# Performance work log

Measured on AMD Instinct MI355X. Metric: run time of the kernel, lower is better.

The kernel has to match this reference:

```python
import jax, jax.numpy as jnp
import numpy as np

FF = 7    # feature_filter_size
FC = 3    # feature_channel_size
PF = 9    # patch_filter_size
R = 9     # search_radius


def setup_inputs() -> dict:
    key = jax.random.key(0)
    x = jax.random.uniform(key, (1, 384, 384, 3), dtype=jnp.float32)
    # feature filter initialized as in the module: identity delta at center per color
    ff = np.zeros((FF, FF, 3, FC), np.float32)
    c = FF // 2
    for i in range(3):
        ff[c, c, i, i] = 1.0
    pf = np.ones((PF, PF), np.float32)   # patch filter = all ones (box)
    inv_sigma = jnp.ones((1,), jnp.float32)
    return {"x": x,
            "feature_filter": jnp.asarray(ff),
            "patch_filter": jnp.asarray(pf),
            "inv_sigma": inv_sigma}


def _conv_same_edge(img, kern):
    # img [B,H,W,Ci], kern [kh,kw,Ci,Co]; edge-clamped boundary (Halide clamp)
    kh, kw = kern.shape[0], kern.shape[1]
    ph, pw = kh // 2, kw // 2
    p = jnp.pad(img, ((0, 0), (ph, ph), (pw, pw), (0, 0)), mode="edge")
    return jax.lax.conv_general_dilated(
        p, kern, window_strides=(1, 1), padding="VALID",
        dimension_numbers=("NHWC", "HWIO", "NHWC"))


def reference(x, feature_filter, patch_filter, inv_sigma):
    B, H, W, C = x.shape
    fc = feature_filter.shape[-1]
    # 1) learned feature transform of the image
    feat = _conv_same_edge(x, feature_filter)                    # [B,H,W,FC]
    # edge-clamped padded copies for shifted (search-window) reads
    xp = jnp.pad(x,    ((0, 0), (R, R), (R, R), (0, 0)), mode="edge")
    fp = jnp.pad(feat, ((0, 0), (R, R), (R, R), (0, 0)), mode="edge")
    pk = patch_filter[:, :, None, None]                          # [PF,PF,1,1]

    dys, dxs = jnp.meshgrid(jnp.arange(2 * R + 1), jnp.arange(2 * R + 1), indexing="ij")
    offsets = jnp.stack([dys.ravel(), dxs.ravel()], axis=-1)     # [(2R+1)^2, 2]

    def step(carry, off):
        num, den = carry
        dy, dx = off[0], off[1]
        fs = jax.lax.dynamic_slice(fp, (0, dy, dx, 0), (B, H, W, fc))
        xs = jax.lax.dynamic_slice(xp, (0, dy, dx, 0), (B, H, W, C))
        # squared feature distance at this offset
        d2 = jnp.sum((feat - fs) ** 2, axis=-1, keepdims=True)   # [B,H,W,1]
        # patch-filter aggregation of pixelwise distances
        pd = _conv_same_edge(d2, pk)                             # [B,H,W,1]
        w = jnp.exp(-pd * inv_sigma[0])                          # exponential weight
        return (num + w * xs, den + w), None

    init = (jnp.zeros((B, H, W, C), x.dtype), jnp.zeros((B, H, W, 1), x.dtype))
    (num, den), _ = jax.lax.scan(step, init, offsets)
    return num / den
```

## Files before the change

### kernel.cpp

```cpp
#include <hip/hip_runtime.h>

#define Hh 384
#define Ww 384
#define NPX (Hh * Ww)

#define TW 64
#define TH 32
#define NTX 6
#define NTILES 72
#define FHH 58
#define FHW 90
#define OG 64
#define NBLK 768
#define IPB 6
#define VMAX 12
#define CSW 76
#define ROWB (FHW * 8)

typedef _Float16 half_t;
typedef _Float16 __attribute__((ext_vector_type(2))) half2_t;
typedef _Float16 __attribute__((ext_vector_type(4))) half4_t;

__device__ __forceinline__ int iclampi(int v) { return v < 0 ? 0 : (v > 383 ? 383 : v); }

__device__ __forceinline__ half2_t u2h(unsigned u) {
    union { unsigned u; half2_t h; } c; c.u = u; return c.h;
}
__device__ __forceinline__ float fdot2u(unsigned a, half2_t w, float c) {
    return __builtin_amdgcn_fdot2(u2h(a), w, c, false);
}
__device__ __forceinline__ float d2u(unsigned aL, unsigned aH, unsigned bL, unsigned bH) {
    half2_t dl = u2h(aL) - u2h(bL);
    half2_t dh = u2h(aH) - u2h(bH);
    return __builtin_amdgcn_fdot2(dl, dl, __builtin_amdgcn_fdot2(dh, dh, 0.f, false), false);
}

#if __has_builtin(__builtin_amdgcn_exp2f)
__device__ __forceinline__ float exp2fast(float x) { return __builtin_amdgcn_exp2f(x); }
#else
__device__ __forceinline__ float exp2fast(float x) { return __expf(x * 0.69314718055994531f); }
#endif

#define LOG2E 1.4426950408889634f

__global__ __launch_bounds__(256) void k_feat(const float* __restrict__ x,
                                              const float* __restrict__ ff,
                                              const float* __restrict__ pf,
                                              float* __restrict__ feat,
                                              unsigned* __restrict__ wpg) {
    int idx = blockIdx.x * 256 + threadIdx.x;
    int py = idx / Ww, px = idx % Ww;
    float a0 = 0.f, a1 = 0.f, a2 = 0.f;
    for (int i = 0; i < 7; ++i) {
        int yy = iclampi(py + i - 3);
        for (int j = 0; j < 7; ++j) {
            int xx = iclampi(px + j - 3);
            const float* xp = x + (yy * Ww + xx) * 3;
            const float* fp = ff + (i * 7 + j) * 9;
            float v0 = xp[0], v1 = xp[1], v2 = xp[2];
            a0 += v0 * fp[0] + v1 * fp[3] + v2 * fp[6];
            a1 += v0 * fp[1] + v1 * fp[4] + v2 * fp[7];
            a2 += v0 * fp[2] + v1 * fp[5] + v2 * fp[8];
        }
    }
    float* o = feat + idx * 3;
    o[0] = a0; o[1] = a1; o[2] = a2;

    if (blockIdx.x == 0) {
        __shared__ int oks[2];
        int t = threadIdx.x;
        if (t < 54) {
            int i = t / 6, sl = t % 6;
            float a = 0.f, b = 0.f;
            if (sl < 4)      { a = pf[i * 9 + 2 * sl]; b = pf[i * 9 + 2 * sl + 1]; }
            else if (sl == 4){ a = pf[i * 9 + 8]; b = 0.f; }
            else             { a = 0.f; b = pf[i * 9 + 8]; }
            half2_t h = { (half_t)a, (half_t)b };
            union { half2_t h; unsigned u; } c; c.h = h;
            wpg[t] = c.u;
        }
        bool ok = true;
        if (t < 81) ok = (pf[t] == pf[0]);
        unsigned long long bal = __ballot(ok);
        if (t < 128 && (t & 63) == 0) oks[t >> 6] = (~bal) == 0ULL;
        __syncthreads();
        if (t == 0) wpg[63] = (oks[0] && oks[1]) ? 1u : 0u;
    }
}

__global__ __launch_bounds__(256, 3) void k_nlm(const float* __restrict__ x,
                                                const float* __restrict__ feat,
                                                const unsigned* __restrict__ wpg,
                                                const float* __restrict__ pf,
                                                const float* __restrict__ inv_sigma,
                                                half4_t* __restrict__ part) {
    __shared__ half4_t sfT[FHH * FHW];
    __shared__ union {
        float cs[32 * CSW];
        half_t d2g[40 * 72];
    } su;

    const int b = blockIdx.x, tid = threadIdx.x;
    const int tx = tid & 7, ty = tid >> 3;

    if (wpg[63] != 0u) {
        float* s_cs = su.cs;
        const float mExp2 = -pf[0] * inv_sigma[0] * LOG2E;

        const int lane = tid & 63, wv = tid >> 6;
        const int band = (wv < 3) ? wv : (lane >> 3);
        const int c72  = (wv < 3) ? lane : (64 + (lane & 7));
        const int act  = (wv < 3) | (lane < 24);
        const int r0 = band * 12;
        const int nrows = (band < 2) ? 20 : 16;

        float num0[8], num1[8], num2[8], den[8];
        unsigned bbL[20], bbH[20];
        unsigned cbyP[10];
        int ccs = 0;

        float* cswb = s_cs + r0 * CSW + c72;
        const float* csr = s_cs + ty * CSW + 8 * tx;

        int cur_t = -1, oyt = 0, oxt = 0, vslot = 0, xbase = 0;

        for (int it = b * IPB; it < b * IPB + IPB; ++it) {
            int t = it >> 6;
            int g = it & (OG - 1);

            if (t != cur_t) {
                if (cur_t >= 0) {
#pragma unroll
                    for (int k = 0; k < 8; ++k) {
                        int px = (oyt + ty) * Ww + oxt + 8 * tx + k;
                        half4_t h = { (half_t)num0[k], (half_t)num1[k], (half_t)num2[k], (half_t)den[k] };
                        part[(size_t)vslot * NPX + px] = h;
                    }
                }
                cur_t = t;
                int tyi = t / NTX;
                oyt = tyi * TH; oxt = (t - tyi * NTX) * TW;
                vslot = b - (OG * t) / IPB;
                xbase = ((oyt + ty) * Ww + oxt + 8 * tx) * 3;

                __syncthreads();
                for (int e = tid; e < FHH * FHW; e += 256) {
                    int ly = e / FHW, lx = e - ly * FHW;
                    int gy = iclampi(oyt - 13 + ly), gx = iclampi(oxt - 13 + lx);
                    const float* fp = feat + (gy * Ww + gx) * 3;
                    sfT[e] = half4_t{ (half_t)fp[0], (half_t)fp[1], (half_t)fp[2], (half_t)0.f };
                }
                __syncthreads();

                if (act) {
                    ccs = iclampi(oxt + c72 - 4) - oxt + 13;
#pragma unroll
                    for (int i = 0; i < 20; i += 2) {
                        int cA = (iclampi(oyt + r0 + i - 4) - oyt + 13) * ROWB;
                        int cB = (iclampi(oyt + r0 + i - 3) - oyt + 13) * ROWB;
                        cbyP[i >> 1] = (unsigned)cA | ((unsigned)cB << 16);
                        uint2 qA = *(const uint2*)((const char*)sfT + cA + ccs * 8);
                        uint2 qB = *(const uint2*)((const char*)sfT + cB + ccs * 8);
                        bbL[i] = qA.x; bbH[i] = qA.y;
                        bbL[i + 1] = qB.x; bbH[i + 1] = qB.y;
                    }
                }
#pragma unroll
                for (int k = 0; k < 8; ++k) { num0[k] = 0.f; num1[k] = 0.f; num2[k] = 0.f; den[k] = 0.f; }
            }

            int o0 = (361 * g) / OG, o1 = (361 * (g + 1)) / OG;
            for (int o = o0; o < o1; ++o) {
                int oy = o / 19, ox = o - oy * 19;
                int offy = oy - 9, offx = ox - 9;

                __syncthreads();
                if (act) {
                    const char* colp = (const char*)sfT + (ccs + offx) * 8 + offy * ROWB;
                    float ring[9]; float s = 0.f;
#pragma unroll
                    for (int i = 0; i < 20; ++i) {
                        int cb = (i & 1) ? (int)(cbyP[i >> 1] >> 16) : (int)(cbyP[i >> 1] & 0xffffu);
                        uint2 q = *(const uint2*)(colp + cb);
                        float d2v = d2u(q.x, q.y, bbL[i], bbH[i]);
                        ring[i % 9] = d2v;
                        s += d2v;
                        if (i >= 8) {
                            if (i < nrows) cswb[(i - 8) * CSW] = s;
                            s -= ring[(i - 8) % 9];
                        }
                    }
                }
                __syncthreads();

                float4 A = *(const float4*)(csr);
                float4 Bv = *(const float4*)(csr + 4);
                float4 Cv = *(const float4*)(csr + 8);
                float4 Dv = *(const float4*)(csr + 12);
                float w_[16] = { A.x, A.y, A.z, A.w, Bv.x, Bv.y, Bv.z, Bv.w,
                                 Cv.x, Cv.y, Cv.z, Cv.w, Dv.x, Dv.y, Dv.z, Dv.w };
                float pdv[8];
                pdv[0] = w_[0] + w_[1] + w_[2] + w_[3] + w_[4] + w_[5] + w_[6] + w_[7] + w_[8];
#pragma unroll
                for (int k = 1; k < 8; ++k) pdv[k] = pdv[k - 1] - w_[k - 1] + w_[k + 8];

                int safe = ((unsigned)(oyt + offy) <= (unsigned)(Hh - TH)) &
                           ((unsigned)(oxt + offx) <= (unsigned)(Ww - TW));
                if (safe) {
                    const float* xp = x + xbase + (offy * Ww + offx) * 3;
#pragma unroll
                    for (int k = 0; k < 8; ++k) {
                        float wgt = exp2fast(pdv[k] * mExp2);
                        num0[k] += wgt * xp[3 * k + 0];
                        num1[k] += wgt * xp[3 * k + 1];
                        num2[k] += wgt * xp[3 * k + 2];
                        den[k] += wgt;
                    }
                } else {
                    int ry = iclampi(oyt + ty + offy);
                    const float* xr = x + ry * (Ww * 3);
#pragma unroll
                    for (int k = 0; k < 8; ++k) {
                        float wgt = exp2fast(pdv[k] * mExp2);
                        int gx = iclampi(oxt + 8 * tx + k + offx);
                        const float* xq = xr + gx * 3;
                        num0[k] += wgt * xq[0];
                        num1[k] += wgt * xq[1];
                        num2[k] += wgt * xq[2];
                        den[k] += wgt;
                    }
                }
            }
        }

#pragma unroll
        for (int k = 0; k < 8; ++k) {
            int px = (oyt + ty) * Ww + oxt + 8 * tx + k;
            half4_t h = { (half_t)num0[k], (half_t)num1[k], (half_t)num2[k], (half_t)den[k] };
            part[(size_t)vslot * NPX + px] = h;
        }
    } else {
        half_t* sd2g = su.d2g;
        const float isig2 = inv_sigma[0] * LOG2E;

        float num0[8], num1[8], num2[8], den[8];
        int bidx[12]; unsigned fbL[12], fbH[12];
        int cur_t = -1, oyt = 0, oxt = 0, vslot = 0;

        for (int it = b * IPB; it < b * IPB + IPB; ++it) {
            int t = it >> 6;
            int g = it & (OG - 1);

            if (t != cur_t) {
                if (cur_t >= 0) {
#pragma unroll
                    for (int k = 0; k < 8; ++k) {
                        int px = (oyt + ty) * Ww + oxt + 8 * tx + k;
                        half4_t h = { (half_t)num0[k], (half_t)num1[k], (half_t)num2[k], (half_t)den[k] };
                        part[(size_t)vslot * NPX + px] = h;
                    }
                }
                cur_t = t;
                int tyi = t / NTX;
                oyt = tyi * TH; oxt = (t - tyi * NTX) * TW;
                vslot = b - (OG * t) / IPB;

                __syncthreads();
                for (int e = tid; e < FHH * FHW; e += 256) {
                    int ly = e / FHW, lx = e - ly * FHW;
                    int gy = iclampi(oyt - 13 + ly), gx = iclampi(oxt - 13 + lx);
                    const float* fp = feat + (gy * Ww + gx) * 3;
                    sfT[e] = half4_t{ (half_t)fp[0], (half_t)fp[1], (half_t)fp[2], (half_t)0.f };
                }
                __syncthreads();

#pragma unroll
                for (int s = 0; s < 12; ++s) {
                    int e = tid + s * 256;
                    if (e < 40 * 72) {
                        int r = e / 72, cc = e - r * 72;
                        int ri = iclampi(oyt - 4 + r) - oyt + 13;
                        int ci = iclampi(oxt - 4 + cc) - oxt + 13;
                        bidx[s] = ri * FHW + ci;
                        uint2 q = *(const uint2*)&sfT[bidx[s]];
                        fbL[s] = q.x; fbH[s] = q.y;
                    } else { bidx[s] = 0; fbL[s] = 0; fbH[s] = 0; }
                }
#pragma unroll
                for (int k = 0; k < 8; ++k) { num0[k] = 0.f; num1[k] = 0.f; num2[k] = 0.f; den[k] = 0.f; }
            }

            int o0 = (361 * g) / OG, o1 = (361 * (g + 1)) / OG;
            for (int o = o0; o < o1; ++o) {
                int oy = o / 19, ox = o - oy * 19;
                int offy = oy - 9, offx = ox - 9;
                int du = offy * FHW + offx;

                __syncthreads();
#pragma unroll
                for (int s = 0; s < 12; ++s) {
                    int e = tid + s * 256;
                    if (e < 40 * 72) {
                        uint2 q = *(const uint2*)&sfT[bidx[s] + du];
                        sd2g[e] = (half_t)d2u(fbL[s], fbH[s], q.x, q.y);
                    }
                }
                __syncthreads();

                float pd[8];
#pragma unroll
                for (int k = 0; k < 8; ++k) pd[k] = 0.f;
#pragma unroll
                for (int i = 0; i < 9; ++i) {
                    const uint4* rp = (const uint4*)&sd2g[(ty + i) * 72 + 8 * tx];
                    uint4 Aq = rp[0], Bq = rp[1];
                    unsigned rr[8] = { Aq.x, Aq.y, Aq.z, Aq.w, Bq.x, Bq.y, Bq.z, Bq.w };
                    unsigned sh[7];
#pragma unroll
                    for (int m = 0; m < 7; ++m) sh[m] = __builtin_amdgcn_alignbit(rr[m + 1], rr[m], 16);
                    half2_t w0 = u2h(wpg[i * 6 + 0]), w1 = u2h(wpg[i * 6 + 1]);
                    half2_t w2 = u2h(wpg[i * 6 + 2]), w3 = u2h(wpg[i * 6 + 3]);
                    half2_t wtE = u2h(wpg[i * 6 + 4]), wtO = u2h(wpg[i * 6 + 5]);
#pragma unroll
                    for (int k = 0; k < 8; k += 2) {
                        int m = k >> 1;
                        float p = pd[k];
                        p = fdot2u(rr[m + 0], w0, p);
                        p = fdot2u(rr[m + 1], w1, p);
                        p = fdot2u(rr[m + 2], w2, p);
                        p = fdot2u(rr[m + 3], w3, p);
                        p = fdot2u(rr[m + 4], wtE, p);
                        pd[k] = p;
                        float q = pd[k + 1];
                        q = fdot2u(sh[m + 0], w0, q);
                        q = fdot2u(sh[m + 1], w1, q);
                        q = fdot2u(sh[m + 2], w2, q);
                        q = fdot2u(sh[m + 3], w3, q);
                        q = fdot2u(rr[m + 4], wtO, q);
                        pd[k + 1] = q;
                    }
                }

                int ry = iclampi(oyt + ty + offy);
                const float* xr = x + ry * (Ww * 3);
#pragma unroll
                for (int k = 0; k < 8; ++k) {
                    float wgt = exp2fast(-pd[k] * isig2);
                    int gx = iclampi(oxt + 8 * tx + k + offx);
                    const float* xq = xr + gx * 3;
                    num0[k] += wgt * xq[0];
                    num1[k] += wgt * xq[1];
                    num2[k] += wgt * xq[2];
                    den[k] += wgt;
                }
            }
        }

#pragma unroll
        for (int k = 0; k < 8; ++k) {
            int px = (oyt + ty) * Ww + oxt + 8 * tx + k;
            half4_t h = { (half_t)num0[k], (half_t)num1[k], (half_t)num2[k], (half_t)den[k] };
            part[(size_t)vslot * NPX + px] = h;
        }
    }
}

__global__ __launch_bounds__(256) void k_reduce(const half4_t* __restrict__ part,
                                                float* __restrict__ out) {
    int px = blockIdx.x * 256 + threadIdx.x;
    if (px >= NPX) return;
    int y = px / Ww, xx = px - y * Ww;
    int t = (y / TH) * NTX + xx / TW;
    int bfirst = (OG * t) / IPB;
    int blast = (OG * t + OG - 1) / IPB;
    int nvis = blast - bfirst + 1;
    float n0 = 0.f, n1 = 0.f, n2 = 0.f, dd = 0.f;
#pragma unroll
    for (int v = 0; v < VMAX; ++v) {
        if (v < nvis) {
            half4_t h = part[(size_t)v * NPX + px];
            n0 += (float)h.x; n1 += (float)h.y; n2 += (float)h.z; dd += (float)h.w;
        }
    }
    float inv = 1.f / dd;
    out[px * 3 + 0] = n0 * inv;
    out[px * 3 + 1] = n1 * inv;
    out[px * 3 + 2] = n2 * inv;
}

extern "C" void kernel_launch(void* const* d_in, const int* in_sizes, int n_in,
                              void* d_out, int out_size, void* d_ws, size_t ws_size,
                              hipStream_t stream) {
    const float* x    = (const float*)d_in[0];
    const float* ff   = (const float*)d_in[1];
    const float* pf   = (const float*)d_in[2];
    const float* isig = (const float*)d_in[3];
    float* out = (float*)d_out;

    float* feat   = (float*)d_ws;
    unsigned* wpg = (unsigned*)((char*)d_ws + (size_t)NPX * 3 * 4);
    half4_t* part = (half4_t*)((char*)d_ws + (size_t)NPX * 3 * 4 + 256);

    k_feat<<<dim3(NPX / 256), 256, 0, stream>>>(x, ff, pf, feat, wpg);
    k_nlm<<<dim3(NBLK), 256, 0, stream>>>(x, feat, wpg, pf, isig, part);
    k_reduce<<<dim3((NPX + 255) / 256), 256, 0, stream>>>(part, out);
}
```

Baseline: 101.6 us.

## Split shared feature tile into SoA half2+half arrays and raise occupancy

Replaces the padded half4 feature tile in shared memory with separate arrays: one half2 array for channels 0-1 and one half array for channel 2. Shared memory per block drops from 8 to 6 bytes per element, and launch bounds go from 3 to 4 blocks per CU to gain occupancy. The column-sum stride changes to 74, which forces the float4 reads to become float2 reads. The cost is two LDS loads per distance instead of one 64-bit load, plus a separate scalar fp16 multiply for the third channel, and possibly register pressure under the tighter bound.

```diff
diff --git a/kernel.cpp b/kernel.cpp
--- a/kernel.cpp
+++ b/kernel.cpp
@@ -14,8 +14,8 @@
 #define NBLK 768
 #define IPB 6
 #define VMAX 12
-#define CSW 76
-#define ROWB (FHW * 8)
+#define CSW 74
+#define ROWA (FHW * 4)
 
 typedef _Float16 half_t;
 typedef _Float16 __attribute__((ext_vector_type(2))) half2_t;
@@ -29,10 +29,11 @@
 __device__ __forceinline__ float fdot2u(unsigned a, half2_t w, float c) {
     return __builtin_amdgcn_fdot2(u2h(a), w, c, false);
 }
-__device__ __forceinline__ float d2u(unsigned aL, unsigned aH, unsigned bL, unsigned bH) {
-    half2_t dl = u2h(aL) - u2h(bL);
-    half2_t dh = u2h(aH) - u2h(bH);
-    return __builtin_amdgcn_fdot2(dl, dl, __builtin_amdgcn_fdot2(dh, dh, 0.f, false), false);
+__device__ __forceinline__ float d2soa(unsigned aA, half_t aB, unsigned bA, half_t bB) {
+    half2_t d01 = u2h(aA) - u2h(bA);
+    half_t dc2 = aB - bB;
+    float c2 = (float)dc2 * (float)dc2;
+    return __builtin_amdgcn_fdot2(d01, d01, c2, false);
 }
 
 #if __has_builtin(__builtin_amdgcn_exp2f)
@@ -88,14 +89,15 @@
     }
 }
 
-__global__ __launch_bounds__(256, 3) void k_nlm(const float* __restrict__ x,
+__global__ __launch_bounds__(256, 4) void k_nlm(const float* __restrict__ x,
                                                 const float* __restrict__ feat,
                                                 const unsigned* __restrict__ wpg,
                                                 const float* __restrict__ pf,
                                                 const float* __restrict__ inv_sigma,
                                                 half4_t* __restrict__ part) {
-    __shared__ half4_t sfT[FHH * FHW];
-    __shared__ union {
+    __shared__ __align__(16) unsigned sfA[FHH * FHW];
+    __shared__ __align__(16) half_t   sfB[FHH * FHW];
+    __shared__ __align__(16) union {
         float cs[32 * CSW];
         half_t d2g[40 * 72];
     } su;
@@ -115,7 +117,7 @@
         const int nrows = (band < 2) ? 20 : 16;
 
         float num0[8], num1[8], num2[8], den[8];
-        unsigned bbL[20], bbH[20];
+        unsigned bbA[20]; half_t bbB[20];
         unsigned cbyP[10];
         int ccs = 0;
 
@@ -148,7 +150,10 @@
                     int ly = e / FHW, lx = e - ly * FHW;
                     int gy = iclampi(oyt - 13 + ly), gx = iclampi(oxt - 13 + lx);
                     const float* fp = feat + (gy * Ww + gx) * 3;
-                    sfT[e] = half4_t{ (half_t)fp[0], (half_t)fp[1], (half_t)fp[2], (half_t)0.f };
+                    half2_t h01 = { (half_t)fp[0], (half_t)fp[1] };
+                    union { half2_t h; unsigned u; } c; c.h = h01;
+                    sfA[e] = c.u;
+                    sfB[e] = (half_t)fp[2];
                 }
                 __syncthreads();
 
@@ -156,13 +161,13 @@
                     ccs = iclampi(oxt + c72 - 4) - oxt + 13;
 #pragma unroll
                     for (int i = 0; i < 20; i += 2) {
-                        int cA = (iclampi(oyt + r0 + i - 4) - oyt + 13) * ROWB;
-                        int cB = (iclampi(oyt + r0 + i - 3) - oyt + 13) * ROWB;
+                        int cA = (iclampi(oyt + r0 + i - 4) - oyt + 13) * ROWA;
+                        int cB = (iclampi(oyt + r0 + i - 3) - oyt + 13) * ROWA;
                         cbyP[i >> 1] = (unsigned)cA | ((unsigned)cB << 16);
-                        uint2 qA = *(const uint2*)((const char*)sfT + cA + ccs * 8);
-                        uint2 qB = *(const uint2*)((const char*)sfT + cB + ccs * 8);
-                        bbL[i] = qA.x; bbH[i] = qA.y;
-                        bbL[i + 1] = qB.x; bbH[i + 1] = qB.y;
+                        bbA[i]     = *(const unsigned*)((const char*)sfA + cA + ccs * 4);
+                        bbB[i]     = *(const half_t*)((const char*)sfB + (cA >> 1) + ccs * 2);
+                        bbA[i + 1] = *(const unsigned*)((const char*)sfA + cB + ccs * 4);
+                        bbB[i + 1] = *(const half_t*)((const char*)sfB + (cB >> 1) + ccs * 2);
                     }
                 }
 #pragma unroll
@@ -176,13 +181,15 @@
 
                 __syncthreads();
                 if (act) {
-                    const char* colp = (const char*)sfT + (ccs + offx) * 8 + offy * ROWB;
+                    const char* colpA = (const char*)sfA + (ccs + offx) * 4 + offy * ROWA;
+                    const char* colpB = (const char*)sfB + (ccs + offx) * 2 + offy * (ROWA / 2);
                     float ring[9]; float s = 0.f;
 #pragma unroll
                     for (int i = 0; i < 20; ++i) {
                         int cb = (i & 1) ? (int)(cbyP[i >> 1] >> 16) : (int)(cbyP[i >> 1] & 0xffffu);
-                        uint2 q = *(const uint2*)(colp + cb);
-                        float d2v = d2u(q.x, q.y, bbL[i], bbH[i]);
+                        unsigned qa = *(const unsigned*)(colpA + cb);
+                        half_t  qb = *(const half_t*)(colpB + (cb >> 1));
+                        float d2v = d2soa(qa, qb, bbA[i], bbB[i]);
                         ring[i % 9] = d2v;
                         s += d2v;
                         if (i >= 8) {
@@ -193,12 +200,16 @@
                 }
                 __syncthreads();
 
-                float4 A = *(const float4*)(csr);
-                float4 Bv = *(const float4*)(csr + 4);
-                float4 Cv = *(const float4*)(csr + 8);
-                float4 Dv = *(const float4*)(csr + 12);
-                float w_[16] = { A.x, A.y, A.z, A.w, Bv.x, Bv.y, Bv.z, Bv.w,
-                                 Cv.x, Cv.y, Cv.z, Cv.w, Dv.x, Dv.y, Dv.z, Dv.w };
+                float2 q0 = *(const float2*)(csr);
+                float2 q1 = *(const float2*)(csr + 2);
+                float2 q2 = *(const float2*)(csr + 4);
+                float2 q3 = *(const float2*)(csr + 6);
+                float2 q4 = *(const float2*)(csr + 8);
+                float2 q5 = *(const float2*)(csr + 10);
+                float2 q6 = *(const float2*)(csr + 12);
+                float2 q7 = *(const float2*)(csr + 14);
+                float w_[16] = { q0.x, q0.y, q1.x, q1.y, q2.x, q2.y, q3.x, q3.y,
+                                 q4.x, q4.y, q5.x, q5.y, q6.x, q6.y, q7.x, q7.y };
                 float pdv[8];
                 pdv[0] = w_[0] + w_[1] + w_[2] + w_[3] + w_[4] + w_[5] + w_[6] + w_[7] + w_[8];
 #pragma unroll
@@ -244,7 +255,7 @@
         const float isig2 = inv_sigma[0] * LOG2E;
 
         float num0[8], num1[8], num2[8], den[8];
-        int bidx[12]; unsigned fbL[12], fbH[12];
+        int bidx[12]; unsigned fbA[12]; half_t fbB[12];
         int cur_t = -1, oyt = 0, oxt = 0, vslot = 0;
 
         for (int it = b * IPB; it < b * IPB + IPB; ++it) {
@@ -270,7 +281,10 @@
                     int ly = e / FHW, lx = e - ly * FHW;
                     int gy = iclampi(oyt - 13 + ly), gx = iclampi(oxt - 13 + lx);
                     const float* fp = feat + (gy * Ww + gx) * 3;
-                    sfT[e] = half4_t{ (half_t)fp[0], (half_t)fp[1], (half_t)fp[2], (half_t)0.f };
+                    half2_t h01 = { (half_t)fp[0], (half_t)fp[1] };
+                    union { half2_t h; unsigned u; } c; c.h = h01;
+                    sfA[e] = c.u;
+                    sfB[e] = (half_t)fp[2];
                 }
                 __syncthreads();
 
@@ -282,9 +296,9 @@
                         int ri = iclampi(oyt - 4 + r) - oyt + 13;
                         int ci = iclampi(oxt - 4 + cc) - oxt + 13;
                         bidx[s] = ri * FHW + ci;
-                        uint2 q = *(const uint2*)&sfT[bidx[s]];
-                        fbL[s] = q.x; fbH[s] = q.y;
-                    } else { bidx[s] = 0; fbL[s] = 0; fbH[s] = 0; }
+                        fbA[s] = sfA[bidx[s]];
+                        fbB[s] = sfB[bidx[s]];
+                    } else { bidx[s] = 0; fbA[s] = 0; fbB[s] = (half_t)0.f; }
                 }
 #pragma unroll
                 for (int k = 0; k < 8; ++k) { num0[k] = 0.f; num1[k] = 0.f; num2[k] = 0.f; den[k] = 0.f; }
@@ -301,8 +315,9 @@
                 for (int s = 0; s < 12; ++s) {
                     int e = tid + s * 256;
                     if (e < 40 * 72) {
-                        uint2 q = *(const uint2*)&sfT[bidx[s] + du];
-                        sd2g[e] = (half_t)d2u(fbL[s], fbH[s], q.x, q.y);
+                        unsigned qa = sfA[bidx[s] + du];
+                        half_t  qb = sfB[bidx[s] + du];
+                        sd2g[e] = (half_t)d2soa(qa, qb, fbA[s], fbB[s]);
                     }
                 }
                 __syncthreads();
```

New measurement: 277.7 us. 2.73x slower.
